# Performance work log

Hardware: AMD Instinct MI355X
Metric: run time of the kernel (lower is better)

## Reference

```python
import jax, jax.numpy as jnp
import numpy as np

# Brevitas-style fake quantization:
#  - Int8ActPerTensorFloat: signed, symmetric, per-tensor float scale, range [-128, 127]
#  - 4-bit weight, narrow range: [-7, 7]
#  - Int32Bias: quantized at scale s_in * s_w
# Scales are taken from per-tensor abs-max statistics (brevitas stats-based init).

def _round(v):
    return jnp.round(v)

def _fake_quant(v, scale, qmin, qmax):
    return jnp.clip(_round(v / scale), qmin, qmax) * scale


def setup_inputs() -> dict:
    key = jax.random.key(0)
    k1, k2, k3 = jax.random.split(key, 3)
    x = jax.random.normal(k1, (16, 3, 224, 224), dtype=jnp.float32)
    W = jax.random.normal(k2, (128, 3, 3, 3), dtype=jnp.float32) * 0.1
    b = jax.random.normal(k3, (128,), dtype=jnp.float32) * 0.01
    return {"x": x, "W": W, "b": b}


def reference(x, W, b):
    EPS = 1e-8
    # input quant: int8 per-tensor
    s_in = jnp.maximum(jnp.max(jnp.abs(x)) / 127.0, EPS)
    x_q = _fake_quant(x, s_in, -128.0, 127.0)
    # weight quant: 4-bit narrow-range per-tensor
    s_w = jnp.maximum(jnp.max(jnp.abs(W)) / 7.0, EPS)
    w_q = _fake_quant(W, s_w, -7.0, 7.0)
    # bias quant: int32 at scale s_in * s_w
    s_b = s_in * s_w
    b_q = _fake_quant(b, s_b, -2147483648.0, 2147483647.0)
    # conv2d, NCHW x OIHW -> NCHW, stride 1, valid padding (torch default padding=0)
    y = jax.lax.conv_general_dilated(
        x_q, w_q, window_strides=(1, 1), padding="VALID",
        dimension_numbers=("NCHW", "OIHW", "NCHW"))
    y = y + b_q[None, :, None, None]
    # output quant: int8 per-tensor
    s_out = jnp.maximum(jnp.max(jnp.abs(y)) / 127.0, EPS)
    y_q = _fake_quant(y, s_out, -128.0, 127.0)
    return y_q
```

## Files before the change

### kernel.cpp

```cpp
#include <hip/hip_runtime.h>
#include <stdint.h>

typedef int v4i __attribute__((ext_vector_type(4)));

#define QEPS 1e-8f


__global__ void k_init(unsigned int* s) { if (threadIdx.x < 4) s[threadIdx.x] = 0u; }

__global__ __launch_bounds__(256) void k_absmax(
    const float4* __restrict__ x, int n4, unsigned int* __restrict__ s) {
  __shared__ unsigned int red[256];
  const int t = threadIdx.x;
  unsigned int m = 0u;
  const int i = blockIdx.x * 256 + t;
  if (i < n4) {
    float4 v = x[i];
    m =        __float_as_uint(v.x) & 0x7fffffffu;
    m = max(m, __float_as_uint(v.y) & 0x7fffffffu);
    m = max(m, __float_as_uint(v.z) & 0x7fffffffu);
    m = max(m, __float_as_uint(v.w) & 0x7fffffffu);
  }
  red[t] = m;
  __syncthreads();
  for (int off = 128; off > 0; off >>= 1) {
    if (t < off) red[t] = max(red[t], red[t + off]);
    __syncthreads();
  }
  if (t == 0) atomicMax(&s[0], red[0]);
}

__global__ __launch_bounds__(128) void k_prep(
    const float* __restrict__ W, const float* __restrict__ b,
    unsigned int* __restrict__ s, int* __restrict__ wB, float* __restrict__ qb) {
  __shared__ float red[128];
  const int t = threadIdx.x;
  float w27[27];
  float m = 0.0f;
  #pragma unroll
  for (int k = 0; k < 27; ++k) { w27[k] = W[t * 27 + k]; m = fmaxf(m, fabsf(w27[k])); }
  red[t] = m;
  __syncthreads();
  for (int off = 64; off > 0; off >>= 1) {
    if (t < off) red[t] = fmaxf(red[t], red[t + off]);
    __syncthreads();
  }
  const float wmax = red[0];
  if (t == 0) s[1] = __float_as_uint(wmax);
  const float s_w  = fmaxf(wmax / 7.0f, QEPS);
  const float s_in = fmaxf(__uint_as_float(s[0]) / 127.0f, QEPS);

  int q[27];
  #pragma unroll
  for (int k = 0; k < 27; ++k) {
    float v = rintf(w27[k] / s_w);
    q[k] = (int)fminf(fmaxf(v, -7.0f), 7.0f);
  }
  #pragma unroll
  for (int qd = 0; qd < 4; ++qd) {
    #pragma unroll
    for (int w = 0; w < 4; ++w) {
      int word = 0;
      #pragma unroll
      for (int bi = 0; bi < 4; ++bi) {
        const int j = 4 * w + bi;
        const int val = (qd < 3 && j < 9) ? q[j * 3 + qd] : 0;
        word |= (val & 0xff) << (8 * bi);
      }
      wB[t * 16 + qd * 4 + w] = word;
    }
  }
  qb[t] = rintf(b[t] / (s_in * s_w));
}

template<int PASS>
__global__ __launch_bounds__(256, 3) void k_conv(
    const float* __restrict__ x, const int* __restrict__ wB,
    const float* __restrict__ qb, float* __restrict__ out,
    unsigned int* __restrict__ s) {
  __shared__ __align__(16) int xcol[132 * 4];
  __shared__ int redi[256];

  const int t = threadIdx.x;
  const int owt = blockIdx.x & 1;
  const int r2 = blockIdx.x >> 1;
  const int n  = r2 & 15;
  const int oh = r2 >> 4;
  const int ow0 = owt * 128;

  const float s_in = fmaxf(__uint_as_float(s[0]) / 127.0f, QEPS);

  if (t < 131) {
    const int gcol = ow0 + t;
    int qv[9];
    if (gcol < 224) {
      #pragma unroll
      for (int r = 0; r < 9; ++r) {
        const int c = r / 3, kh = r - c * 3;
        const float xv = x[((n * 3 + c) * 224 + (oh + kh)) * 224 + gcol];
        qv[r] = (int)fminf(fmaxf(rintf(xv / s_in), -128.0f), 127.0f);
      }
    } else {
      #pragma unroll
      for (int r = 0; r < 9; ++r) qv[r] = 0;
    }
    const int w0 = (qv[0] & 0xff) | (qv[1] & 0xff) << 8 | (qv[2] & 0xff) << 16 | (qv[3] & 0xff) << 24;
    const int w1 = (qv[4] & 0xff) | (qv[5] & 0xff) << 8 | (qv[6] & 0xff) << 16 | (qv[7] & 0xff) << 24;
    const int w2 = (qv[8] & 0xff);
    ((v4i*)xcol)[t] = (v4i){w0, w1, w2, 0};
  }

  const int lane = t & 63;
  const int wv   = t >> 6;
  const int l15  = lane & 15;
  const int quad = lane >> 4;

  v4i bfr[8];
  int qbi[8];
  #pragma unroll
  for (int nt = 0; nt < 8; ++nt) {
    bfr[nt] = ((const v4i*)wB)[(nt * 16 + l15) * 4 + quad];
    qbi[nt] = (int)qb[nt * 16 + l15];
  }

  __syncthreads();

  v4i afr[2];
  #pragma unroll
  for (int mt = 0; mt < 2; ++mt)
    afr[mt] = ((const v4i*)xcol)[(2 * wv + mt) * 16 + l15 + quad];

  v4i acc[2][8];
  #pragma unroll
  for (int mt = 0; mt < 2; ++mt)
    #pragma unroll
    for (int nt = 0; nt < 8; ++nt) acc[mt][nt] = (v4i){0, 0, 0, 0};

  #pragma unroll
  for (int mt = 0; mt < 2; ++mt)
    #pragma unroll
    for (int nt = 0; nt < 8; ++nt)
      acc[mt][nt] = __builtin_amdgcn_mfma_i32_16x16x64_i8(afr[mt], bfr[nt], acc[mt][nt], 0, 0, 0);

  if (PASS == 0) {
    int vm = 0;
    #pragma unroll
    for (int mt = 0; mt < 2; ++mt) {
      const int owb = ow0 + (2 * wv + mt) * 16 + quad * 4;
      #pragma unroll
      for (int nt = 0; nt < 8; ++nt) {
        #pragma unroll
        for (int r = 0; r < 4; ++r) {
          if (owb + r < 222) {
            const int v = acc[mt][nt][r] + qbi[nt];
            vm = max(vm, v < 0 ? -v : v);
          }
        }
      }
    }
    redi[t] = vm;
    __syncthreads();
    for (int off = 128; off > 0; off >>= 1) {
      if (t < off) redi[t] = max(redi[t], redi[t + off]);
      __syncthreads();
    }
    if (t == 0) atomicMax(&s[2], (unsigned int)redi[0]);
  } else {
    const int vmax = (int)s[2];
    const float s_w  = fmaxf(__uint_as_float(s[1]) / 7.0f, QEPS);
    const float s_b  = s_in * s_w;
    const float s_out = fmaxf((s_b * (float)vmax) / 127.0f, QEPS);
    const float h = s_b / s_out;
    #pragma unroll
    for (int mt = 0; mt < 2; ++mt) {
      const int owb = ow0 + (2 * wv + mt) * 16 + quad * 4;
      if (owb < 222) {
        #pragma unroll
        for (int nt = 0; nt < 8; ++nt) {
          const int oc = nt * 16 + l15;
          float o4[4];
          #pragma unroll
          for (int r = 0; r < 4; ++r) {
            const float vf = (float)(acc[mt][nt][r] + qbi[nt]);
            float q = rintf(vf * h);
            q = fminf(fmaxf(q, -128.0f), 127.0f);
            o4[r] = q * s_out;
          }
          float* p = out + ((n * 128 + oc) * 49284 + oh * 222 + owb);
          *(float2*)p = make_float2(o4[0], o4[1]);
          if (owb + 2 < 222) *(float2*)(p + 2) = make_float2(o4[2], o4[3]);
        }
      }
    }
  }
}

extern "C" void kernel_launch(void* const* d_in, const int* in_sizes, int n_in,
                              void* d_out, int out_size, void* d_ws, size_t ws_size,
                              hipStream_t stream) {
  const float* x = (const float*)d_in[0];
  const float* W = (const float*)d_in[1];
  const float* b = (const float*)d_in[2];
  float* out = (float*)d_out;

  unsigned int* s = (unsigned int*)d_ws;
  int*   wB = (int*)((char*)d_ws + 256);
  float* qb = (float*)((char*)d_ws + 256 + 8192);

  k_init<<<1, 64, 0, stream>>>(s);

  const int n4 = in_sizes[0] / 4;
  k_absmax<<<(n4 + 255) / 256, 256, 0, stream>>>((const float4*)x, n4, s);

  k_prep<<<1, 128, 0, stream>>>(W, b, s, wB, qb);

  const int nblk = 2 * 16 * 222;
  k_conv<0><<<nblk, 256, 0, stream>>>(x, wB, qb, out, s);
  k_conv<1><<<nblk, 256, 0, stream>>>(x, wB, qb, out, s);
}
```

Measured before the change: 666.9 us.

## Process three output rows per block with double-buffered im2col staging

Each conv block now computes three consecutive output rows instead of one, cutting the grid threefold. The im2col tile goes into a two-slot shared buffer, so the next row's global loads and quantization can overlap the current row's MFMAs. Even rows use aligned float4 stores, and the per-block setup (weight fragments, bias, scales, absmax reduction) is amortized over more work. The cost is fewer blocks to fill the GPU (2368 per pass), and input rows are still reloaded across the 3x3 window.

```diff
diff --git a/kernel.cpp b/kernel.cpp
--- a/kernel.cpp
+++ b/kernel.cpp
@@ -78,37 +78,17 @@
     const float* __restrict__ x, const int* __restrict__ wB,
     const float* __restrict__ qb, float* __restrict__ out,
     unsigned int* __restrict__ s) {
-  __shared__ __align__(16) int xcol[132 * 4];
+  __shared__ __align__(16) int xcol[2][132 * 4];
   __shared__ int redi[256];
 
   const int t = threadIdx.x;
   const int owt = blockIdx.x & 1;
   const int r2 = blockIdx.x >> 1;
   const int n  = r2 & 15;
-  const int oh = r2 >> 4;
+  const int oh0 = (r2 >> 4) * 3;
   const int ow0 = owt * 128;
 
   const float s_in = fmaxf(__uint_as_float(s[0]) / 127.0f, QEPS);
-
-  if (t < 131) {
-    const int gcol = ow0 + t;
-    int qv[9];
-    if (gcol < 224) {
-      #pragma unroll
-      for (int r = 0; r < 9; ++r) {
-        const int c = r / 3, kh = r - c * 3;
-        const float xv = x[((n * 3 + c) * 224 + (oh + kh)) * 224 + gcol];
-        qv[r] = (int)fminf(fmaxf(rintf(xv / s_in), -128.0f), 127.0f);
-      }
-    } else {
-      #pragma unroll
-      for (int r = 0; r < 9; ++r) qv[r] = 0;
-    }
-    const int w0 = (qv[0] & 0xff) | (qv[1] & 0xff) << 8 | (qv[2] & 0xff) << 16 | (qv[3] & 0xff) << 24;
-    const int w1 = (qv[4] & 0xff) | (qv[5] & 0xff) << 8 | (qv[6] & 0xff) << 16 | (qv[7] & 0xff) << 24;
-    const int w2 = (qv[8] & 0xff);
-    ((v4i*)xcol)[t] = (v4i){w0, w1, w2, 0};
-  }
 
   const int lane = t & 63;
   const int wv   = t >> 6;
@@ -123,41 +103,119 @@
     qbi[nt] = (int)qb[nt * 16 + l15];
   }
 
-  __syncthreads();
-
-  v4i afr[2];
-  #pragma unroll
-  for (int mt = 0; mt < 2; ++mt)
-    afr[mt] = ((const v4i*)xcol)[(2 * wv + mt) * 16 + l15 + quad];
-
-  v4i acc[2][8];
-  #pragma unroll
-  for (int mt = 0; mt < 2; ++mt)
-    #pragma unroll
-    for (int nt = 0; nt < 8; ++nt) acc[mt][nt] = (v4i){0, 0, 0, 0};
-
-  #pragma unroll
-  for (int mt = 0; mt < 2; ++mt)
-    #pragma unroll
-    for (int nt = 0; nt < 8; ++nt)
-      acc[mt][nt] = __builtin_amdgcn_mfma_i32_16x16x64_i8(afr[mt], bfr[nt], acc[mt][nt], 0, 0, 0);
-
-  if (PASS == 0) {
-    int vm = 0;
-    #pragma unroll
-    for (int mt = 0; mt < 2; ++mt) {
-      const int owb = ow0 + (2 * wv + mt) * 16 + quad * 4;
-      #pragma unroll
-      for (int nt = 0; nt < 8; ++nt) {
+  float s_out = 1.0f, h = 1.0f;
+  if (PASS == 1) {
+    const int vmax = (int)s[2];
+    const float s_w = fmaxf(__uint_as_float(s[1]) / 7.0f, QEPS);
+    const float s_b = s_in * s_w;
+    s_out = fmaxf((s_b * (float)vmax) / 127.0f, QEPS);
+    h = s_b / s_out;
+  }
+
+  auto stage = [&](int oh, int buf) {
+    if (t < 131) {
+      const int gcol = ow0 + t;
+      int qv[9];
+      if (gcol < 224) {
         #pragma unroll
-        for (int r = 0; r < 4; ++r) {
-          if (owb + r < 222) {
-            const int v = acc[mt][nt][r] + qbi[nt];
-            vm = max(vm, v < 0 ? -v : v);
+        for (int r = 0; r < 9; ++r) {
+          const int c = r / 3, kh = r - c * 3;
+          const float xv = x[((n * 3 + c) * 224 + (oh + kh)) * 224 + gcol];
+          qv[r] = (int)fminf(fmaxf(rintf(xv / s_in), -128.0f), 127.0f);
+        }
+      } else {
+        #pragma unroll
+        for (int r = 0; r < 9; ++r) qv[r] = 0;
+      }
+      const int w0 = (qv[0] & 0xff) | (qv[1] & 0xff) << 8 | (qv[2] & 0xff) << 16 | (qv[3] & 0xff) << 24;
+      const int w1 = (qv[4] & 0xff) | (qv[5] & 0xff) << 8 | (qv[6] & 0xff) << 16 | (qv[7] & 0xff) << 24;
+      const int w2 = (qv[8] & 0xff);
+      ((v4i*)xcol[buf])[t] = (v4i){w0, w1, w2, 0};
+    }
+  };
+
+  stage(oh0, 0);
+
+  int vm = 0;
+
+  #pragma unroll
+  for (int j = 0; j < 3; ++j) {
+    __syncthreads();
+    if (j < 2) stage(oh0 + j + 1, (j + 1) & 1);
+    const int oh = oh0 + j;
+    const int buf = j & 1;
+
+    v4i afr[2];
+    #pragma unroll
+    for (int mt = 0; mt < 2; ++mt)
+      afr[mt] = ((const v4i*)xcol[buf])[(2 * wv + mt) * 16 + l15 + quad];
+
+    v4i acc[2][8];
+    #pragma unroll
+    for (int mt = 0; mt < 2; ++mt)
+      #pragma unroll
+      for (int nt = 0; nt < 8; ++nt) acc[mt][nt] = (v4i){0, 0, 0, 0};
+
+    #pragma unroll
+    for (int mt = 0; mt < 2; ++mt)
+      #pragma unroll
+      for (int nt = 0; nt < 8; ++nt)
+        acc[mt][nt] = __builtin_amdgcn_mfma_i32_16x16x64_i8(afr[mt], bfr[nt], acc[mt][nt], 0, 0, 0);
+
+    if (PASS == 0) {
+      #pragma unroll
+      for (int mt = 0; mt < 2; ++mt) {
+        const int owb = ow0 + (2 * wv + mt) * 16 + quad * 4;
+        const int vv = 222 - owb;
+        if (vv > 0) {
+          #pragma unroll
+          for (int nt = 0; nt < 8; ++nt) {
+            #pragma unroll
+            for (int r = 0; r < 4; ++r) {
+              if (r < vv) {
+                const int v = acc[mt][nt][r] + qbi[nt];
+                vm = max(vm, v < 0 ? -v : v);
+              }
+            }
           }
         }
       }
-    }
+    } else {
+      #pragma unroll
+      for (int mt = 0; mt < 2; ++mt) {
+        const int owb = ow0 + (2 * wv + mt) * 16 + quad * 4;
+        const int vv = 222 - owb;
+        if (vv > 0) {
+          #pragma unroll
+          for (int nt = 0; nt < 8; ++nt) {
+            const int oc = nt * 16 + l15;
+            float o4[4];
+            #pragma unroll
+            for (int r = 0; r < 4; ++r) {
+              const float vf = (float)(acc[mt][nt][r] + qbi[nt]);
+              float q = rintf(vf * h);
+              q = fminf(fmaxf(q, -128.0f), 127.0f);
+              o4[r] = q * s_out;
+            }
+            float* p = out + ((n * 128 + oc) * 49284 + oh * 222 + owb);
+            if (vv >= 4) {
+              if ((oh & 1) == 0) {
+                *(float4*)p = make_float4(o4[0], o4[1], o4[2], o4[3]);
+              } else {
+                *(float2*)p       = make_float2(o4[0], o4[1]);
+                *(float2*)(p + 2) = make_float2(o4[2], o4[3]);
+              }
+            } else {
+              *(float2*)p = make_float2(o4[0], o4[1]);
+            }
+          }
+        }
+      }
+    }
+  }
+
+  if (PASS == 0) {
+    __syncthreads();
     redi[t] = vm;
     __syncthreads();
     for (int off = 128; off > 0; off >>= 1) {
@@ -165,33 +223,6 @@
       __syncthreads();
     }
     if (t == 0) atomicMax(&s[2], (unsigned int)redi[0]);
-  } else {
-    const int vmax = (int)s[2];
-    const float s_w  = fmaxf(__uint_as_float(s[1]) / 7.0f, QEPS);
-    const float s_b  = s_in * s_w;
-    const float s_out = fmaxf((s_b * (float)vmax) / 127.0f, QEPS);
-    const float h = s_b / s_out;
-    #pragma unroll
-    for (int mt = 0; mt < 2; ++mt) {
-      const int owb = ow0 + (2 * wv + mt) * 16 + quad * 4;
-      if (owb < 222) {
-        #pragma unroll
-        for (int nt = 0; nt < 8; ++nt) {
-          const int oc = nt * 16 + l15;
-          float o4[4];
-          #pragma unroll
-          for (int r = 0; r < 4; ++r) {
-            const float vf = (float)(acc[mt][nt][r] + qbi[nt]);
-            float q = rintf(vf * h);
-            q = fminf(fmaxf(q, -128.0f), 127.0f);
-            o4[r] = q * s_out;
-          }
-          float* p = out + ((n * 128 + oc) * 49284 + oh * 222 + owb);
-          *(float2*)p = make_float2(o4[0], o4[1]);
-          if (owb + 2 < 222) *(float2*)(p + 2) = make_float2(o4[2], o4[3]);
-        }
-      }
-    }
   }
 }
 
@@ -214,7 +245,7 @@
 
   k_prep<<<1, 128, 0, stream>>>(W, b, s, wB, qb);
 
-  const int nblk = 2 * 16 * 222;
+  const int nblk = 2 * 16 * 74;
   k_conv<0><<<nblk, 256, 0, stream>>>(x, wB, qb, out, s);
   k_conv<1><<<nblk, 256, 0, stream>>>(x, wB, qb, out, s);
 }
```

Measured after the change: 658.6 us. No clear change (-1.2%).
